# Performance work log

Measured on AMD Instinct MI355X. Metric: run time of the kernel, lower is better.

Reference implementation:

```python
import jax, jax.numpy as jnp
import numpy as np

N = 50000      # num_nodes
R = 32         # num_relations
H = 16         # hidden channels
C = 16         # num_classes
E = 1600000    # num_edges (avg degree 32)


def setup_inputs() -> dict:
    key = jax.random.key(0)
    ks = jax.random.split(key, 8)
    edge_index = jax.random.randint(ks[0], (2, E), 0, N)
    edge_type = jnp.sort(jax.random.randint(ks[1], (E,), 0, R))
    # per-relation [start, end) slices into the sorted edge list (is_sorted=True)
    starts = jnp.searchsorted(edge_type, jnp.arange(R))
    ends = jnp.searchsorted(edge_type, jnp.arange(R) + 1)
    tensor_slice = jnp.stack([starts, ends], axis=1)
    s = 0.05
    W1 = jax.random.normal(ks[2], (R, N, H), dtype=jnp.float32) * s   # layer-1 per-relation embedding (x=None)
    root1 = jax.random.normal(ks[3], (N, H), dtype=jnp.float32) * s  # root weight acts as embedding when x=None
    bias1 = jax.random.normal(ks[4], (H,), dtype=jnp.float32) * s
    W2 = jax.random.normal(ks[5], (R, H, C), dtype=jnp.float32) * s
    root2 = jax.random.normal(ks[6], (H, C), dtype=jnp.float32) * s
    bias2 = jax.random.normal(ks[7], (C,), dtype=jnp.float32) * s
    return {"edge_index": edge_index, "edge_type": edge_type, "tensor_slice": tensor_slice,
            "W1": W1, "root1": root1, "bias1": bias1,
            "W2": W2, "root2": root2, "bias2": bias2}


def reference(edge_index, edge_type, tensor_slice, W1, root1, bias1, W2, root2, bias2):
    src, dst = edge_index[0], edge_index[1]
    # ---- layer 1: x=None, so per-relation transform is an embedding lookup W1[r][src]
    msg1 = W1[edge_type, src]                                        # [E, H] relation-indexed gather
    h1 = root1 + jax.ops.segment_sum(msg1, dst, num_segments=N) + bias1
    h1 = jax.nn.relu(h1)
    # ---- layer 2: transform all nodes per relation once, then gather per edge
    t = jnp.einsum('nh,rhc->rnc', h1, W2)                            # [R, N, C]
    msg2 = t[edge_type, src]                                         # [E, C]
    h2 = h1 @ root2 + jax.ops.segment_sum(msg2, dst, num_segments=N) + bias2
    return jax.nn.log_softmax(h2, axis=1)
```

## Files before the change

kernel.cpp:

```cpp
#include <hip/hip_runtime.h>
#include <hip/hip_bf16.h>

static constexpr int H = 16;
static constexpr int C = 16;

typedef __attribute__((ext_vector_type(8))) short bf16x8;
typedef __attribute__((ext_vector_type(4))) float f32x4;

static __device__ inline unsigned short f2bf(float x) {
    __hip_bfloat16 b = __float2bfloat16(x);
    return *reinterpret_cast<unsigned short*>(&b);
}
static __device__ inline float bflo(unsigned u) { return __uint_as_float(u << 16); }
static __device__ inline float bfhi(unsigned u) { return __uint_as_float(u & 0xffff0000u); }
static __device__ inline void pk_atomic_bf16(unsigned short* addr, unsigned pk) {
    asm volatile("global_atomic_pk_add_bf16 %0, %1, off" :: "v"(addr), "v"(pk) : "memory");
}

__global__ void k1_scatter(const int* __restrict__ srcv, const int* __restrict__ dstv,
                           const int* __restrict__ etv, const float* __restrict__ W1,
                           unsigned short* __restrict__ acc1, int E, int N) {
    int t = blockIdx.x * blockDim.x + threadIdx.x;
    int g = t >> 3;
    int cp = t & 7;
    int e0 = g << 3;
    if (e0 >= E) return;
    int n = min(8, E - e0);
    int s[8], d[8], r[8];
#pragma unroll
    for (int i = 0; i < 8; ++i) {
        int e = e0 + ((i < n) ? i : 0);
        s[i] = srcv[e]; d[i] = dstv[e]; r[i] = etv[e];
    }
    float2 v[8];
#pragma unroll
    for (int i = 0; i < 8; ++i)
        v[i] = *(const float2*)(W1 + ((size_t)r[i] * N + (size_t)s[i]) * H + (cp << 1));
#pragma unroll
    for (int i = 0; i < 8; ++i)
        if (i < n) {
            unsigned pk = ((unsigned)f2bf(v[i].y) << 16) | f2bf(v[i].x);
            pk_atomic_bf16(acc1 + ((size_t)d[i] << 4) + (cp << 1), pk);
        }
}

__global__ void k2_fin1(const float* __restrict__ root1, const float* __restrict__ bias1,
                        const unsigned short* __restrict__ acc1,
                        unsigned int* __restrict__ h1bf, int total4) {
    int i = blockIdx.x * blockDim.x + threadIdx.x;
    if (i >= total4) return;
    float4 rv = ((const float4*)root1)[i];
    uint2 av = ((const uint2*)acc1)[i];
    float4 bv = ((const float4*)bias1)[i & 3];
    float4 o;
    o.x = fmaxf(rv.x + bflo(av.x) + bv.x, 0.0f);
    o.y = fmaxf(rv.y + bfhi(av.x) + bv.y, 0.0f);
    o.z = fmaxf(rv.z + bflo(av.y) + bv.z, 0.0f);
    o.w = fmaxf(rv.w + bfhi(av.y) + bv.w, 0.0f);
    uint2 p;
    p.x = ((unsigned)f2bf(o.y) << 16) | f2bf(o.x);
    p.y = ((unsigned)f2bf(o.w) << 16) | f2bf(o.z);
    ((uint2*)h1bf)[i] = p;
}

__global__ void k0_prep(const int* __restrict__ ts, int* __restrict__ chunk_off, int R) {
    if (blockIdx.x == 0 && threadIdx.x == 0) {
        int acc = 0;
        for (int r = 0; r < R; ++r) {
            chunk_off[r] = acc;
            int cnt = ts[2 * r + 1] - ts[2 * r];
            acc += (cnt + 15) >> 4;
        }
        chunk_off[R] = acc;
    }
}

__global__ void k0_chunkmap(const int* __restrict__ ts, const int* __restrict__ chunk_off,
                            int* __restrict__ cmap_e0, int* __restrict__ cmap_rn,
                            int R, int UB) {
    int c = blockIdx.x * blockDim.x + threadIdx.x;
    if (c >= UB) return;
    int T = chunk_off[R];
    if (c >= T) return;
    int lo = 0, hi = R;
    while (hi - lo > 1) {
        int mid = (lo + hi) >> 1;
        if (chunk_off[mid] <= c) lo = mid; else hi = mid;
    }
    int r = lo;
    int e0 = ts[2 * r] + ((c - chunk_off[r]) << 4);
    int n = min(16, ts[2 * r + 1] - e0);
    cmap_e0[c] = e0;
    cmap_rn[c] = (n << 8) | r;
}

__global__ void k0_cast(const float* __restrict__ W2, unsigned short* __restrict__ w2t,
                        int total ) {
    int i = blockIdx.x * blockDim.x + threadIdx.x;
    if (i >= total) return;
    int r = i >> 8;
    int kc = i & 255;
    int k = kc >> 4;
    int c = kc & 15;
    w2t[(r << 8) + (c << 4) + k] = f2bf(W2[i]);
}

__global__ void k3_mfma(const int* __restrict__ srcv, const int* __restrict__ dstv,
                        const int* __restrict__ cmap_e0, const int* __restrict__ cmap_rn,
                        const int* __restrict__ chunk_off,
                        const unsigned short* __restrict__ h1bf,
                        const unsigned short* __restrict__ w2t,
                        unsigned short* __restrict__ acc2, int R) {
    int w = (blockIdx.x * blockDim.x + threadIdx.x) >> 6;
    int l = threadIdx.x & 63;
    int T = chunk_off[R];
    int c0 = w << 2;
    if (c0 >= T) return;

    int rowA = l & 15;
    int kg = l >> 4;

    int e0[4], rr[4], nn[4], s[4], dd[4];
#pragma unroll
    for (int q = 0; q < 4; ++q) {
        int cq = c0 + q;
        bool ok = cq < T;
        int e = ok ? cmap_e0[cq] : 0;
        int rn = ok ? cmap_rn[cq] : 0;
        e0[q] = e;
        rr[q] = rn & 255;
        nn[q] = rn >> 8;
    }
#pragma unroll
    for (int q = 0; q < 4; ++q) {
        int eA = e0[q] + max(0, min(rowA, nn[q] - 1));
        s[q] = srcv[eA];
        dd[q] = dstv[eA];
    }
    bf16x8 a[4], b[4];
#pragma unroll
    for (int q = 0; q < 4; ++q) {
        bf16x8 z = {0, 0, 0, 0, 0, 0, 0, 0};
        a[q] = z; b[q] = z;
        if (kg < 2) {
            a[q] = *(const bf16x8*)(h1bf + ((size_t)s[q] << 4) + (kg << 3));
            b[q] = *(const bf16x8*)(w2t + ((size_t)rr[q] << 8) + (rowA << 4) + (kg << 3));
        }
    }
    f32x4 d[4];
#pragma unroll
    for (int q = 0; q < 4; ++q) {
        f32x4 z4 = {0.f, 0.f, 0.f, 0.f};
        d[q] = __builtin_amdgcn_mfma_f32_16x16x32_bf16(a[q], b[q], z4, 0, 0, 0);
    }
    int c = l & 15;
#pragma unroll
    for (int q = 0; q < 4; ++q) {
#pragma unroll
        for (int j = 0; j < 4; ++j) {
            int row = (kg << 2) + j;
            float o = __shfl_xor(d[q][j], 1);
            int ddv = __shfl(dd[q], row);
            if (((l & 1) == 0) && row < nn[q]) {
                unsigned pk = ((unsigned)f2bf(o) << 16) | f2bf(d[q][j]);
                pk_atomic_bf16(acc2 + ((size_t)ddv << 4) + c, pk);
            }
        }
    }
}

__global__ void k4_fin2(const unsigned short* __restrict__ h1bf,
                        const unsigned short* __restrict__ acc2,
                        const float* __restrict__ root2, const float* __restrict__ bias2,
                        float* __restrict__ out, int N) {
    int n = blockIdx.x * blockDim.x + threadIdx.x;
    if (n >= N) return;
    const uint4* hp = (const uint4*)(h1bf + (size_t)n * 16);
    uint4 h0 = hp[0], h1 = hp[1];
    float h[16] = {bflo(h0.x), bfhi(h0.x), bflo(h0.y), bfhi(h0.y),
                   bflo(h0.z), bfhi(h0.z), bflo(h0.w), bfhi(h0.w),
                   bflo(h1.x), bfhi(h1.x), bflo(h1.y), bfhi(h1.y),
                   bflo(h1.z), bfhi(h1.z), bflo(h1.w), bfhi(h1.w)};
    const uint4* ap = (const uint4*)(acc2 + (size_t)n * 16);
    uint4 a0 = ap[0], a1 = ap[1];
    float av[16] = {bflo(a0.x), bfhi(a0.x), bflo(a0.y), bfhi(a0.y),
                    bflo(a0.z), bfhi(a0.z), bflo(a0.w), bfhi(a0.w),
                    bflo(a1.x), bfhi(a1.x), bflo(a1.y), bfhi(a1.y),
                    bflo(a1.z), bfhi(a1.z), bflo(a1.w), bfhi(a1.w)};
    float* o = out + (size_t)n * C;
    float z[16];
#pragma unroll
    for (int c = 0; c < 16; ++c) {
        float acc = av[c] + bias2[c];
#pragma unroll
        for (int k = 0; k < 16; ++k) acc += h[k] * root2[k * C + c];
        z[c] = acc;
    }
    float m = z[0];
#pragma unroll
    for (int c = 1; c < 16; ++c) m = fmaxf(m, z[c]);
    float se = 0.f;
#pragma unroll
    for (int c = 0; c < 16; ++c) se += __expf(z[c] - m);
    float lse = m + __logf(se);
#pragma unroll
    for (int c = 0; c < 16; ++c) o[c] = z[c] - lse;
}

extern "C" void kernel_launch(void* const* d_in, const int* in_sizes, int n_in,
                              void* d_out, int out_size, void* d_ws, size_t ws_size,
                              hipStream_t stream) {
    const int*   edge_index   = (const int*)d_in[0];
    const int*   edge_type    = (const int*)d_in[1];
    const int*   tensor_slice = (const int*)d_in[2];
    const float* W1    = (const float*)d_in[3];
    const float* root1 = (const float*)d_in[4];
    const float* bias1 = (const float*)d_in[5];
    const float* W2    = (const float*)d_in[6];
    const float* root2 = (const float*)d_in[7];
    const float* bias2 = (const float*)d_in[8];
    float* out = (float*)d_out;

    const int E = in_sizes[0] / 2;
    const int N = in_sizes[4] / H;
    const int R = in_sizes[2] / 2;
    const int* srcv = edge_index;
    const int* dstv = edge_index + E;

    const int UB = (E + 15) / 16 + R;
    char* p = (char*)d_ws;
    unsigned short* acc1 = (unsigned short*)p;   p += (size_t)N * 16 * 2;
    unsigned short* h1bf = (unsigned short*)p;   p += (size_t)N * 16 * 2;
    unsigned short* w2t = (unsigned short*)p;    p += (size_t)R * 256 * 2;
    unsigned short* acc2 = (unsigned short*)p;   p += (size_t)N * 16 * 2;
    int* chunk_off = (int*)p;                    p += (size_t)(R + 1) * 4;
    p = (char*)(((uintptr_t)p + 15) & ~(uintptr_t)15);
    int* cmap_e0 = (int*)p;                      p += (size_t)UB * 4;
    int* cmap_rn = (int*)p;

    hipMemsetAsync(acc1, 0, (size_t)N * 16 * 2, stream);
    hipMemsetAsync(acc2, 0, (size_t)N * 16 * 2, stream);

    const int B = 256;
    k0_prep<<<1, 64, 0, stream>>>(tensor_slice, chunk_off, R);
    k0_chunkmap<<<(UB + B - 1) / B, B, 0, stream>>>(tensor_slice, chunk_off,
                                                    cmap_e0, cmap_rn, R, UB);
    k0_cast<<<(R * 256 + B - 1) / B, B, 0, stream>>>(W2, w2t, R * 256);
    long long g1 = ((long long)E + 7) / 8;
    long long t1 = g1 * 8;
    k1_scatter<<<(int)((t1 + B - 1) / B), B, 0, stream>>>(srcv, dstv, edge_type, W1, acc1, E, N);
    int total4 = N * H / 4;
    k2_fin1<<<(total4 + B - 1) / B, B, 0, stream>>>(root1, bias1, acc1,
                                                    (unsigned int*)h1bf, total4);
    long long waves = ((long long)UB + 3) / 4;
    long long thr = waves * 64;
    k3_mfma<<<(int)((thr + B - 1) / B), B, 0, stream>>>(srcv, dstv, cmap_e0, cmap_rn,
                                                        chunk_off, h1bf, w2t, acc2, R);
    k4_fin2<<<(N + B - 1) / B, B, 0, stream>>>(h1bf, acc2, root2, bias2, out, N);
}
```

Baseline: 192.6 us.

## Fuse prep kernels and memsets, widen layer-1 scatter to float4 loads

Folds the two memsets, the chunk-offset prep, chunk map and W2 cast into one fused prep kernel. Each chunk-map thread now does a linear scan over relations instead of reading precomputed offsets. The intent is fewer launches and less serialised prep work. The layer-1 scatter now uses 4 threads per edge group with float4 W1 loads and int4 index loads, halving the thread count. Scheduling barriers are added in the MFMA kernel to group its loads. The k3 kernel now bounds by UB instead of the true chunk count, relying on zeroed padding entries (n=0) in the chunk map.

```diff
diff --git a/kernel.cpp b/kernel.cpp
--- a/kernel.cpp
+++ b/kernel.cpp
@@ -17,31 +17,90 @@
     asm volatile("global_atomic_pk_add_bf16 %0, %1, off" :: "v"(addr), "v"(pk) : "memory");
 }
 
+__global__ void k0_fused(const float* __restrict__ W2, const int* __restrict__ ts,
+                         unsigned short* __restrict__ w2t, uint4* __restrict__ zbase,
+                         int* __restrict__ cmap_e0, int* __restrict__ cmap_rn,
+                         int N, int R, int UB) {
+    int t = blockIdx.x * blockDim.x + threadIdx.x;
+    int nz = 4 * N;
+    if (t < nz) {
+        zbase[t] = make_uint4(0u, 0u, 0u, 0u);
+        return;
+    }
+    t -= nz;
+    if (t < R * 256) {
+        int r = t >> 8;
+        int kc = t & 255;
+        int k = kc >> 4, c = kc & 15;
+        w2t[(r << 8) + (c << 4) + k] = f2bf(W2[t]);
+        return;
+    }
+    t -= R * 256;
+    if (t >= UB) return;
+    int cacc = 0, my_e0 = 0, my_rn = 0;
+    for (int r = 0; r < R; ++r) {
+        int b = ts[2 * r], e = ts[2 * r + 1];
+        int nc = (e - b + 15) >> 4;
+        if (t >= cacc && t < cacc + nc) {
+            int e0 = b + ((t - cacc) << 4);
+            my_e0 = e0;
+            my_rn = (min(16, e - e0) << 8) | r;
+        }
+        cacc += nc;
+    }
+    cmap_e0[t] = my_e0;
+    cmap_rn[t] = my_rn;
+}
+
+static __device__ inline void k1_body(const float* __restrict__ W1,
+                                      unsigned short* __restrict__ acc1,
+                                      const int* s, const int* d, const int* r,
+                                      int n, int q, int N) {
+    float4 v[8];
+#pragma unroll
+    for (int i = 0; i < 8; ++i) {
+        unsigned off = (((unsigned)(r[i] * N + s[i])) << 4) + (q << 2);
+        v[i] = *(const float4*)(W1 + off);
+    }
+    __builtin_amdgcn_sched_barrier(0);
+#pragma unroll
+    for (int i = 0; i < 8; ++i) {
+        if (i < n) {
+            unsigned plo = ((unsigned)f2bf(v[i].y) << 16) | f2bf(v[i].x);
+            unsigned phi = ((unsigned)f2bf(v[i].w) << 16) | f2bf(v[i].z);
+            unsigned short* base = acc1 + ((size_t)d[i] << 4) + (q << 2);
+            pk_atomic_bf16(base, plo);
+            pk_atomic_bf16(base + 2, phi);
+        }
+    }
+}
+
 __global__ void k1_scatter(const int* __restrict__ srcv, const int* __restrict__ dstv,
                            const int* __restrict__ etv, const float* __restrict__ W1,
                            unsigned short* __restrict__ acc1, int E, int N) {
     int t = blockIdx.x * blockDim.x + threadIdx.x;
-    int g = t >> 3;
-    int cp = t & 7;
+    int g = t >> 2;
+    int q = t & 3;
     int e0 = g << 3;
     if (e0 >= E) return;
-    int n = min(8, E - e0);
     int s[8], d[8], r[8];
-#pragma unroll
-    for (int i = 0; i < 8; ++i) {
-        int e = e0 + ((i < n) ? i : 0);
-        s[i] = srcv[e]; d[i] = dstv[e]; r[i] = etv[e];
-    }
-    float2 v[8];
-#pragma unroll
-    for (int i = 0; i < 8; ++i)
-        v[i] = *(const float2*)(W1 + ((size_t)r[i] * N + (size_t)s[i]) * H + (cp << 1));
-#pragma unroll
-    for (int i = 0; i < 8; ++i)
-        if (i < n) {
-            unsigned pk = ((unsigned)f2bf(v[i].y) << 16) | f2bf(v[i].x);
-            pk_atomic_bf16(acc1 + ((size_t)d[i] << 4) + (cp << 1), pk);
-        }
+    if (e0 + 8 <= E) {
+        int4 s0 = *(const int4*)(srcv + e0), s1 = *(const int4*)(srcv + e0 + 4);
+        int4 d0 = *(const int4*)(dstv + e0), d1 = *(const int4*)(dstv + e0 + 4);
+        int4 r0 = *(const int4*)(etv + e0),  r1 = *(const int4*)(etv + e0 + 4);
+        s[0]=s0.x; s[1]=s0.y; s[2]=s0.z; s[3]=s0.w; s[4]=s1.x; s[5]=s1.y; s[6]=s1.z; s[7]=s1.w;
+        d[0]=d0.x; d[1]=d0.y; d[2]=d0.z; d[3]=d0.w; d[4]=d1.x; d[5]=d1.y; d[6]=d1.z; d[7]=d1.w;
+        r[0]=r0.x; r[1]=r0.y; r[2]=r0.z; r[3]=r0.w; r[4]=r1.x; r[5]=r1.y; r[6]=r1.z; r[7]=r1.w;
+        k1_body(W1, acc1, s, d, r, 8, q, N);
+    } else {
+        int n = E - e0;
+#pragma unroll
+        for (int i = 0; i < 8; ++i) {
+            int e = e0 + ((i < n) ? i : 0);
+            s[i] = srcv[e]; d[i] = dstv[e]; r[i] = etv[e];
+        }
+        k1_body(W1, acc1, s, d, r, n, q, N);
+    }
 }
 
 __global__ void k2_fin1(const float* __restrict__ root1, const float* __restrict__ bias1,
@@ -63,80 +122,37 @@
     ((uint2*)h1bf)[i] = p;
 }
 
-__global__ void k0_prep(const int* __restrict__ ts, int* __restrict__ chunk_off, int R) {
-    if (blockIdx.x == 0 && threadIdx.x == 0) {
-        int acc = 0;
-        for (int r = 0; r < R; ++r) {
-            chunk_off[r] = acc;
-            int cnt = ts[2 * r + 1] - ts[2 * r];
-            acc += (cnt + 15) >> 4;
-        }
-        chunk_off[R] = acc;
-    }
-}
-
-__global__ void k0_chunkmap(const int* __restrict__ ts, const int* __restrict__ chunk_off,
-                            int* __restrict__ cmap_e0, int* __restrict__ cmap_rn,
-                            int R, int UB) {
-    int c = blockIdx.x * blockDim.x + threadIdx.x;
-    if (c >= UB) return;
-    int T = chunk_off[R];
-    if (c >= T) return;
-    int lo = 0, hi = R;
-    while (hi - lo > 1) {
-        int mid = (lo + hi) >> 1;
-        if (chunk_off[mid] <= c) lo = mid; else hi = mid;
-    }
-    int r = lo;
-    int e0 = ts[2 * r] + ((c - chunk_off[r]) << 4);
-    int n = min(16, ts[2 * r + 1] - e0);
-    cmap_e0[c] = e0;
-    cmap_rn[c] = (n << 8) | r;
-}
-
-__global__ void k0_cast(const float* __restrict__ W2, unsigned short* __restrict__ w2t,
-                        int total ) {
-    int i = blockIdx.x * blockDim.x + threadIdx.x;
-    if (i >= total) return;
-    int r = i >> 8;
-    int kc = i & 255;
-    int k = kc >> 4;
-    int c = kc & 15;
-    w2t[(r << 8) + (c << 4) + k] = f2bf(W2[i]);
-}
-
 __global__ void k3_mfma(const int* __restrict__ srcv, const int* __restrict__ dstv,
                         const int* __restrict__ cmap_e0, const int* __restrict__ cmap_rn,
-                        const int* __restrict__ chunk_off,
                         const unsigned short* __restrict__ h1bf,
                         const unsigned short* __restrict__ w2t,
-                        unsigned short* __restrict__ acc2, int R) {
+                        unsigned short* __restrict__ acc2, int UB) {
     int w = (blockIdx.x * blockDim.x + threadIdx.x) >> 6;
     int l = threadIdx.x & 63;
-    int T = chunk_off[R];
     int c0 = w << 2;
-    if (c0 >= T) return;
-
+    if (c0 >= UB) return;
     int rowA = l & 15;
     int kg = l >> 4;
 
-    int e0[4], rr[4], nn[4], s[4], dd[4];
+    int e0[4], rr[4], nn[4];
 #pragma unroll
     for (int q = 0; q < 4; ++q) {
         int cq = c0 + q;
-        bool ok = cq < T;
-        int e = ok ? cmap_e0[cq] : 0;
+        bool ok = cq < UB;
+        e0[q] = ok ? cmap_e0[cq] : 0;
         int rn = ok ? cmap_rn[cq] : 0;
-        e0[q] = e;
         rr[q] = rn & 255;
         nn[q] = rn >> 8;
     }
+    __builtin_amdgcn_sched_barrier(0);
+    int s[4], dd[4];
 #pragma unroll
     for (int q = 0; q < 4; ++q) {
         int eA = e0[q] + max(0, min(rowA, nn[q] - 1));
         s[q] = srcv[eA];
         dd[q] = dstv[eA];
     }
+    __builtin_amdgcn_sched_barrier(0);
     bf16x8 a[4], b[4];
 #pragma unroll
     for (int q = 0; q < 4; ++q) {
@@ -147,6 +163,7 @@
             b[q] = *(const bf16x8*)(w2t + ((size_t)rr[q] << 8) + (rowA << 4) + (kg << 3));
         }
     }
+    __builtin_amdgcn_sched_barrier(0);
     f32x4 d[4];
 #pragma unroll
     for (int q = 0; q < 4; ++q) {
@@ -211,8 +228,8 @@
                               void* d_out, int out_size, void* d_ws, size_t ws_size,
                               hipStream_t stream) {
     const int*   edge_index   = (const int*)d_in[0];
+    const int*   tensor_slice = (const int*)d_in[2];
     const int*   edge_type    = (const int*)d_in[1];
-    const int*   tensor_slice = (const int*)d_in[2];
     const float* W1    = (const float*)d_in[3];
     const float* root1 = (const float*)d_in[4];
     const float* bias1 = (const float*)d_in[5];
@@ -230,24 +247,19 @@
     const int UB = (E + 15) / 16 + R;
     char* p = (char*)d_ws;
     unsigned short* acc1 = (unsigned short*)p;   p += (size_t)N * 16 * 2;
+    unsigned short* acc2 = (unsigned short*)p;   p += (size_t)N * 16 * 2;
     unsigned short* h1bf = (unsigned short*)p;   p += (size_t)N * 16 * 2;
     unsigned short* w2t = (unsigned short*)p;    p += (size_t)R * 256 * 2;
-    unsigned short* acc2 = (unsigned short*)p;   p += (size_t)N * 16 * 2;
-    int* chunk_off = (int*)p;                    p += (size_t)(R + 1) * 4;
-    p = (char*)(((uintptr_t)p + 15) & ~(uintptr_t)15);
     int* cmap_e0 = (int*)p;                      p += (size_t)UB * 4;
     int* cmap_rn = (int*)p;
 
-    hipMemsetAsync(acc1, 0, (size_t)N * 16 * 2, stream);
-    hipMemsetAsync(acc2, 0, (size_t)N * 16 * 2, stream);
-
     const int B = 256;
-    k0_prep<<<1, 64, 0, stream>>>(tensor_slice, chunk_off, R);
-    k0_chunkmap<<<(UB + B - 1) / B, B, 0, stream>>>(tensor_slice, chunk_off,
-                                                    cmap_e0, cmap_rn, R, UB);
-    k0_cast<<<(R * 256 + B - 1) / B, B, 0, stream>>>(W2, w2t, R * 256);
+    int prep_threads = 4 * N + R * 256 + UB;
+    k0_fused<<<(prep_threads + B - 1) / B, B, 0, stream>>>(W2, tensor_slice, w2t,
+                                                           (uint4*)acc1, cmap_e0, cmap_rn,
+                                                           N, R, UB);
     long long g1 = ((long long)E + 7) / 8;
-    long long t1 = g1 * 8;
+    long long t1 = g1 * 4;
     k1_scatter<<<(int)((t1 + B - 1) / B), B, 0, stream>>>(srcv, dstv, edge_type, W1, acc1, E, N);
     int total4 = N * H / 4;
     k2_fin1<<<(total4 + B - 1) / B, B, 0, stream>>>(root1, bias1, acc1,
@@ -255,6 +267,6 @@
     long long waves = ((long long)UB + 3) / 4;
     long long thr = waves * 64;
     k3_mfma<<<(int)((thr + B - 1) / B), B, 0, stream>>>(srcv, dstv, cmap_e0, cmap_rn,
-                                                        chunk_off, h1bf, w2t, acc2, R);
+                                                        h1bf, w2t, acc2, UB);
     k4_fin2<<<(N + B - 1) / B, B, 0, stream>>>(h1bf, acc2, root2, bias2, out, N);
 }
```

After: 263.8 us. +37.0%, slower.
